# Kernel tuning notes

Measured on AMD Instinct MI355X. Metric: run time of the kernel, lower is better.

Reference implementation:

```python
import jax, jax.numpy as jnp
import numpy as np

MAX_ITER = 100   # Sinkhorn max iterations (from source)
THRESH = 0.01    # early-exit threshold on mean |r - r0|
EPS = 0.1        # entropic regularization eps


def _sinkhorn(K, u, v):
    """K: [B, M, N], u: [B, M], v: [B, N] -> transport plan T: [B, M, N]."""
    def cond(state):
        r, c, err, i = state
        return jnp.logical_and(i < MAX_ITER, err >= THRESH)

    def body(state):
        r, c, err, i = state
        r0 = r
        r = u / jnp.einsum('bmn,bn->bm', K, c)
        c = v / jnp.einsum('bmn,bm->bn', K, r)
        err = jnp.mean(jnp.abs(r - r0))
        return r, c, err, i + 1

    r0 = jnp.ones_like(u)
    c0 = jnp.ones_like(v)
    err0 = jnp.asarray(jnp.inf, dtype=u.dtype)
    r, c, _, _ = jax.lax.while_loop(cond, body, (r0, c0, err0, jnp.asarray(0)))
    # T = diag(r) K diag(c)
    return r[:, :, None] * c[:, None, :] * K


def setup_inputs() -> dict:
    key = jax.random.key(0)
    k1, k2 = jax.random.split(key)
    M, N, n_cls, D = 65536, 4, 2, 1024
    img = jax.random.normal(k1, (M, 1, D), dtype=jnp.float32)
    txt = jax.random.normal(k2, (N, n_cls, D), dtype=jnp.float32)
    # CLIP-style features are L2-normalized so cosine sim lies in [-1, 1]
    img = img / jnp.linalg.norm(img, axis=-1, keepdims=True)
    txt = txt / jnp.linalg.norm(txt, axis=-1, keepdims=True)
    logit_scale = jnp.ones((1,), dtype=jnp.float32) * jnp.float32(np.log(1 / 0.02))
    return {"image_features": img, "text_features": txt, "logit_scale": logit_scale}


def reference(image_features, text_features, logit_scale):
    M = image_features.shape[0]
    N, n_cls, _ = text_features.shape  # N=4, n_cls=2
    b = image_features.shape[1]        # b=1
    # sim: [M, N, b, n_cls] -> [M, N, b*n_cls] -> [b*n_cls, M, N]
    sim = jnp.einsum('mbd,ncd->mnbc', image_features, text_features)
    sim = sim.reshape(M, N, b * n_cls).transpose(2, 0, 1)
    wdist = 1.0 - sim
    u = jnp.full((b * n_cls, M), 1.0 / M, dtype=sim.dtype)
    v = jnp.full((b * n_cls, N), 1.0 / N, dtype=sim.dtype)
    K = jnp.exp(-wdist / EPS)
    T = jax.lax.stop_gradient(_sinkhorn(K, u, v))  # computed under no_grad in torch
    sim_op = jnp.sum(T * sim, axis=(1, 2)).reshape(b, n_cls)
    return jnp.exp(logit_scale) * sim_op
```

## Files before the change

kernel.cpp:

```cpp
#include <hip/hip_runtime.h>
#include <math.h>


#define TPB 256
#define NBLK 256
#define NV 8
#define DV 256
#define SINK_MAX 100
#define SINK_THRESH 0.01f

__device__ __forceinline__ void grid_barrier(unsigned* bar) {
  __syncthreads();
  if (threadIdx.x == 0) {
    __threadfence();
    unsigned target = __hip_atomic_load(&bar[1], __ATOMIC_RELAXED, __HIP_MEMORY_SCOPE_AGENT) + 1u;
    unsigned arrived = __hip_atomic_fetch_add(&bar[0], 1u, __ATOMIC_ACQ_REL, __HIP_MEMORY_SCOPE_AGENT) + 1u;
    if (arrived == gridDim.x) {
      __hip_atomic_store(&bar[0], 0u, __ATOMIC_RELAXED, __HIP_MEMORY_SCOPE_AGENT);
      __hip_atomic_fetch_add(&bar[1], 1u, __ATOMIC_ACQ_REL, __HIP_MEMORY_SCOPE_AGENT);
    } else {
      while (__hip_atomic_load(&bar[1], __ATOMIC_ACQUIRE, __HIP_MEMORY_SCOPE_AGENT) < target) {
        __builtin_amdgcn_s_sleep(2);
      }
    }
    __threadfence();
  }
  __syncthreads();
}

__global__ __launch_bounds__(TPB) void sinkhorn_fused(
    const float* __restrict__ img, const float* __restrict__ txt,
    const float* __restrict__ ls, float* __restrict__ out,
    unsigned* __restrict__ bar, float* __restrict__ slots)
{
  __shared__ float4 stxt[NV * DV];
  __shared__ float red[4][12];

  const int tid = threadIdx.x;
  const int m = blockIdx.x * TPB + tid;

  const float4* t4 = reinterpret_cast<const float4*>(txt);
  for (int i = tid; i < NV * DV; i += TPB) stxt[i] = t4[i];
  __syncthreads();

  float acc[NV];
  #pragma unroll
  for (int v = 0; v < NV; ++v) acc[v] = 0.f;

  const float4* row = reinterpret_cast<const float4*>(img) + (size_t)m * DV;
  #pragma unroll 4
  for (int j = 0; j < DV; ++j) {
    float4 a = row[j];
    #pragma unroll
    for (int v = 0; v < NV; ++v) {
      float4 t = stxt[v * DV + j];
      acc[v] += a.x * t.x + a.y * t.y + a.z * t.z + a.w * t.w;
    }
  }

  float K[NV];
  #pragma unroll
  for (int v = 0; v < NV; ++v) K[v] = expf(10.f * (acc[v] - 1.f));

  float cvec[NV];
  #pragma unroll
  for (int v = 0; v < NV; ++v) cvec[v] = 1.f;
  float r_prev[2] = {1.f, 1.f};
  float err = INFINITY;
  int it = 0;

  while (it < SINK_MAX && err >= SINK_THRESH) {
    float part[9];
    float errp = 0.f;
    #pragma unroll
    for (int b = 0; b < 2; ++b) {
      float denom = 0.f;
      #pragma unroll
      for (int n = 0; n < 4; ++n) denom += K[n*2+b] * cvec[n*2+b];
      float r = (1.f / 65536.f) / denom;
      errp += fabsf(r - r_prev[b]);
      r_prev[b] = r;
      #pragma unroll
      for (int n = 0; n < 4; ++n) part[1 + b*4 + n] = K[n*2+b] * r;
    }
    part[0] = errp;

    #pragma unroll
    for (int k = 0; k < 9; ++k) {
      float s = part[k];
      #pragma unroll
      for (int off = 1; off < 64; off <<= 1) s += __shfl_xor(s, off, 64);
      if ((tid & 63) == 0) red[tid >> 6][k] = s;
    }
    __syncthreads();
    if (tid < 9) {
      float s = red[0][tid] + red[1][tid] + red[2][tid] + red[3][tid];
      atomicAdd(&slots[it * 9 + tid], s);
    }
    grid_barrier(bar);

    err = __hip_atomic_load(&slots[it * 9 + 0], __ATOMIC_RELAXED, __HIP_MEMORY_SCOPE_AGENT)
          * (1.f / 131072.f);
    #pragma unroll
    for (int b = 0; b < 2; ++b) {
      #pragma unroll
      for (int n = 0; n < 4; ++n) {
        float S = __hip_atomic_load(&slots[it * 9 + 1 + b*4 + n],
                                    __ATOMIC_RELAXED, __HIP_MEMORY_SCOPE_AGENT);
        cvec[n*2+b] = 0.25f / S;
      }
    }
    ++it;
  }

  float op[2];
  #pragma unroll
  for (int b = 0; b < 2; ++b) {
    float s = 0.f;
    #pragma unroll
    for (int n = 0; n < 4; ++n) s += cvec[n*2+b] * K[n*2+b] * acc[n*2+b];
    op[b] = s * r_prev[b];
  }
  #pragma unroll
  for (int k = 0; k < 2; ++k) {
    float s = op[k];
    #pragma unroll
    for (int off = 1; off < 64; off <<= 1) s += __shfl_xor(s, off, 64);
    if ((tid & 63) == 0) red[tid >> 6][k] = s;
  }
  __syncthreads();
  if (tid < 2) {
    float tot = red[0][tid] + red[1][tid] + red[2][tid] + red[3][tid];
    atomicAdd(&out[tid], expf(ls[0]) * tot);
  }
}

extern "C" void kernel_launch(void* const* d_in, const int* in_sizes, int n_in,
                              void* d_out, int out_size, void* d_ws, size_t ws_size,
                              hipStream_t stream) {
  const float* img = (const float*)d_in[0];
  const float* txt = (const float*)d_in[1];
  const float* ls  = (const float*)d_in[2];
  float* out = (float*)d_out;

  hipMemsetAsync(d_out, 0, 2 * sizeof(float), stream);
  hipMemsetAsync(d_ws, 0, 4096, stream);

  unsigned* bar = (unsigned*)d_ws;
  float* slots = (float*)((char*)d_ws + 64);

  sinkhorn_fused<<<NBLK, TPB, 0, stream>>>(img, txt, ls, out, bar, slots);
}
```

Baseline: 470.6 us.

## Split similarity GEMV into a separate high-parallelism kernel before Sinkhorn

Moves the image-text dot products out of the persistent 256-block Sinkhorn kernel into its own kernel with 2048 blocks. In that kernel eight threads cooperate per row with coalesced strided loads and shuffle reductions, and the eight similarities per row are written to workspace. The Sinkhorn kernel then reads these 8 floats per row and runs the same grid-barrier iteration. The aim is to replace the old pattern, where only 256 blocks each streamed one 4 KB row per thread uncoalesced, with a memory-bound pass that better saturates bandwidth. The cost is an extra launch plus a 2 MB workspace round trip, and the fused path is kept as a fallback when the workspace is too small.

```diff
diff --git a/kernel.cpp b/kernel.cpp
--- a/kernel.cpp
+++ b/kernel.cpp
@@ -3,7 +3,8 @@
 
 
 #define TPB 256
-#define NBLK 256
+#define K1_BLOCKS 2048
+#define K2_BLOCKS 256
 #define NV 8
 #define DV 256
 #define SINK_MAX 100
@@ -28,6 +29,143 @@
   __syncthreads();
 }
 
+__global__ __launch_bounds__(TPB) void sim_kernel(
+    const float* __restrict__ img, const float* __restrict__ txt,
+    float4* __restrict__ simout)
+{
+  __shared__ float4 stxt[NV * DV];
+  const int tid = threadIdx.x;
+  const float4* t4 = reinterpret_cast<const float4*>(txt);
+  for (int i = tid; i < NV * DV; i += TPB) stxt[i] = t4[i];
+  __syncthreads();
+
+  const int c = tid & 7;
+  const int row = blockIdx.x * 32 + (tid >> 3);
+  const float4* row4 = reinterpret_cast<const float4*>(img) + (size_t)row * DV;
+
+  float acc[NV];
+  #pragma unroll
+  for (int v = 0; v < NV; ++v) acc[v] = 0.f;
+
+  for (int i0 = 0; i0 < 32; i0 += 8) {
+    float4 a[8];
+    #pragma unroll
+    for (int t = 0; t < 8; ++t) a[t] = row4[c + 8 * (i0 + t)];
+    #pragma unroll
+    for (int t = 0; t < 8; ++t) {
+      const int j = c + 8 * (i0 + t);
+      #pragma unroll
+      for (int v = 0; v < NV; ++v) {
+        float4 tt = stxt[v * DV + j];
+        acc[v] += a[t].x * tt.x + a[t].y * tt.y + a[t].z * tt.z + a[t].w * tt.w;
+      }
+    }
+  }
+
+  #pragma unroll
+  for (int v = 0; v < NV; ++v) {
+    float s = acc[v];
+    s += __shfl_xor(s, 1, 64);
+    s += __shfl_xor(s, 2, 64);
+    s += __shfl_xor(s, 4, 64);
+    acc[v] = s;
+  }
+  if (c == 0) {
+    simout[(size_t)row * 2]     = make_float4(acc[0], acc[1], acc[2], acc[3]);
+    simout[(size_t)row * 2 + 1] = make_float4(acc[4], acc[5], acc[6], acc[7]);
+  }
+}
+
+__global__ __launch_bounds__(TPB) void sinkhorn_kernel(
+    const float4* __restrict__ simout, const float* __restrict__ ls,
+    float* __restrict__ out, unsigned* __restrict__ bar,
+    float* __restrict__ slots)
+{
+  __shared__ float red[4][12];
+  const int tid = threadIdx.x;
+  const int m = blockIdx.x * TPB + tid;
+
+  float4 s0 = simout[(size_t)m * 2];
+  float4 s1 = simout[(size_t)m * 2 + 1];
+  const float sim[NV] = {s0.x, s0.y, s0.z, s0.w, s1.x, s1.y, s1.z, s1.w};
+
+  float K[NV];
+  #pragma unroll
+  for (int v = 0; v < NV; ++v) K[v] = expf(10.f * (sim[v] - 1.f));
+
+  float cvec[NV];
+  #pragma unroll
+  for (int v = 0; v < NV; ++v) cvec[v] = 1.f;
+  float r_prev[2] = {1.f, 1.f};
+  float err = INFINITY;
+  int it = 0;
+
+  while (it < SINK_MAX && err >= SINK_THRESH) {
+    float part[9];
+    float errp = 0.f;
+    #pragma unroll
+    for (int b = 0; b < 2; ++b) {
+      float denom = 0.f;
+      #pragma unroll
+      for (int n = 0; n < 4; ++n) denom += K[n*2+b] * cvec[n*2+b];
+      float r = (1.f / 65536.f) / denom;
+      errp += fabsf(r - r_prev[b]);
+      r_prev[b] = r;
+      #pragma unroll
+      for (int n = 0; n < 4; ++n) part[1 + b*4 + n] = K[n*2+b] * r;
+    }
+    part[0] = errp;
+
+    #pragma unroll
+    for (int k = 0; k < 9; ++k) {
+      float s = part[k];
+      #pragma unroll
+      for (int off = 1; off < 64; off <<= 1) s += __shfl_xor(s, off, 64);
+      if ((tid & 63) == 0) red[tid >> 6][k] = s;
+    }
+    __syncthreads();
+    if (tid < 9) {
+      float s = red[0][tid] + red[1][tid] + red[2][tid] + red[3][tid];
+      atomicAdd(&slots[it * 9 + tid], s);
+    }
+    grid_barrier(bar);
+
+    err = __hip_atomic_load(&slots[it * 9 + 0], __ATOMIC_RELAXED, __HIP_MEMORY_SCOPE_AGENT)
+          * (1.f / 131072.f);
+    #pragma unroll
+    for (int b = 0; b < 2; ++b) {
+      #pragma unroll
+      for (int n = 0; n < 4; ++n) {
+        float S = __hip_atomic_load(&slots[it * 9 + 1 + b*4 + n],
+                                    __ATOMIC_RELAXED, __HIP_MEMORY_SCOPE_AGENT);
+        cvec[n*2+b] = 0.25f / S;
+      }
+    }
+    ++it;
+  }
+
+  float op[2];
+  #pragma unroll
+  for (int b = 0; b < 2; ++b) {
+    float s = 0.f;
+    #pragma unroll
+    for (int n = 0; n < 4; ++n) s += cvec[n*2+b] * K[n*2+b] * sim[n*2+b];
+    op[b] = s * r_prev[b];
+  }
+  #pragma unroll
+  for (int k = 0; k < 2; ++k) {
+    float s = op[k];
+    #pragma unroll
+    for (int off = 1; off < 64; off <<= 1) s += __shfl_xor(s, off, 64);
+    if ((tid & 63) == 0) red[tid >> 6][k] = s;
+  }
+  __syncthreads();
+  if (tid < 2) {
+    float tot = red[0][tid] + red[1][tid] + red[2][tid] + red[3][tid];
+    atomicAdd(&out[tid], expf(ls[0]) * tot);
+  }
+}
+
 __global__ __launch_bounds__(TPB) void sinkhorn_fused(
     const float* __restrict__ img, const float* __restrict__ txt,
     const float* __restrict__ ls, float* __restrict__ out,
@@ -35,7 +173,6 @@
 {
   __shared__ float4 stxt[NV * DV];
   __shared__ float red[4][12];
-
   const int tid = threadIdx.x;
   const int m = blockIdx.x * TPB + tid;
 
@@ -46,7 +183,6 @@
   float acc[NV];
   #pragma unroll
   for (int v = 0; v < NV; ++v) acc[v] = 0.f;
-
   const float4* row = reinterpret_cast<const float4*>(img) + (size_t)m * DV;
   #pragma unroll 4
   for (int j = 0; j < DV; ++j) {
@@ -57,18 +193,15 @@
       acc[v] += a.x * t.x + a.y * t.y + a.z * t.z + a.w * t.w;
     }
   }
-
   float K[NV];
   #pragma unroll
   for (int v = 0; v < NV; ++v) K[v] = expf(10.f * (acc[v] - 1.f));
-
   float cvec[NV];
   #pragma unroll
   for (int v = 0; v < NV; ++v) cvec[v] = 1.f;
   float r_prev[2] = {1.f, 1.f};
   float err = INFINITY;
   int it = 0;
-
   while (it < SINK_MAX && err >= SINK_THRESH) {
     float part[9];
     float errp = 0.f;
@@ -84,7 +217,6 @@
       for (int n = 0; n < 4; ++n) part[1 + b*4 + n] = K[n*2+b] * r;
     }
     part[0] = errp;
-
     #pragma unroll
     for (int k = 0; k < 9; ++k) {
       float s = part[k];
@@ -98,7 +230,6 @@
       atomicAdd(&slots[it * 9 + tid], s);
     }
     grid_barrier(bar);
-
     err = __hip_atomic_load(&slots[it * 9 + 0], __ATOMIC_RELAXED, __HIP_MEMORY_SCOPE_AGENT)
           * (1.f / 131072.f);
     #pragma unroll
@@ -112,7 +243,6 @@
     }
     ++it;
   }
-
   float op[2];
   #pragma unroll
   for (int b = 0; b < 2; ++b) {
@@ -148,6 +278,13 @@
 
   unsigned* bar = (unsigned*)d_ws;
   float* slots = (float*)((char*)d_ws + 64);
-
-  sinkhorn_fused<<<NBLK, TPB, 0, stream>>>(img, txt, ls, out, bar, slots);
-}
+  float4* sim8 = (float4*)((char*)d_ws + 4096);
+
+  const size_t need = 4096 + (size_t)65536 * 8 * sizeof(float);
+  if (ws_size >= need) {
+    sim_kernel<<<K1_BLOCKS, TPB, 0, stream>>>(img, txt, sim8);
+    sinkhorn_kernel<<<K2_BLOCKS, TPB, 0, stream>>>(sim8, ls, out, bar, slots);
+  } else {
+    sinkhorn_fused<<<K2_BLOCKS, TPB, 0, stream>>>(img, txt, ls, out, bar, slots);
+  }
+}
```

Measured after the change: 442.5 us. -6.0%, faster.
